# Performance work log

Hardware: AMD Instinct MI355X
Metric: run time of the kernel (lower is better)

The kernel has to match this reference:

```python
import jax, jax.numpy as jnp
import numpy as np
from jax import lax

TEMP = 65.0
CLIP_DIST = 0.01
EPS = 1e-6  # torch PairwiseDistance eps (added to the difference) and log eps
NTOKEN, NINP, NHID = 32000, 1024, 1024
SEQ_LEN, BSZ, NSAMPLES = 128, 64, 10


def setup_inputs() -> dict:
    key = jax.random.key(0)
    ks = jax.random.split(key, 7)
    data = jax.random.randint(ks[0], (SEQ_LEN, BSZ), 0, NTOKEN)
    samples = jax.random.randint(ks[1], (NSAMPLES, SEQ_LEN * BSZ), 0, NTOKEN)
    # encoder init_weights: uniform(-0.1, 0.1); RNN weights small to avoid tanh saturation
    emb_W = jax.random.uniform(ks[2], (NTOKEN, NINP), minval=-0.1, maxval=0.1, dtype=jnp.float32)
    W_ih = jax.random.normal(ks[3], (NHID, NINP), dtype=jnp.float32) * 0.03
    b_ih = jax.random.normal(ks[4], (NHID,), dtype=jnp.float32) * 0.01
    W_hh = jax.random.normal(ks[5], (NHID, NHID), dtype=jnp.float32) * 0.03
    b_hh = jax.random.normal(ks[6], (NHID,), dtype=jnp.float32) * 0.01
    return {"data": data, "samples": samples, "emb_W": emb_W,
            "W_ih": W_ih, "b_ih": b_ih, "W_hh": W_hh, "b_hh": b_hh}


def _sq_pdist(x, y):
    # torch PairwiseDistance(p=2).pow(2): ||x - y + eps||^2 (no sqrt needed)
    d = x - y + EPS
    return jnp.sum(d * d, axis=-1)


def reference(data, samples, emb_W, W_ih, b_ih, W_hh, b_hh):
    seq_len, bsz = data.shape
    nhid = W_hh.shape[0]
    emb = emb_W[data]                                  # [S, B, ninp]
    h0 = jnp.zeros((bsz, nhid), dtype=emb_W.dtype)

    def step(h, e):
        h_new = jnp.tanh(e @ W_ih.T + b_ih + h @ W_hh.T + b_hh)
        return h_new, h_new

    _, outs = lax.scan(step, h0, emb)                  # [S, B, H]
    raw = jnp.concatenate([h0[None], outs], axis=0)    # [S+1, B, H]

    # positive term: temp * ||h_t - h_{t+1}||^2, summed, averaged over seq_len
    pos = TEMP * _sq_pdist(raw[:-1], raw[1:])          # [S, B]
    loss = pos.sum() / seq_len

    prev = raw[:-1].reshape(seq_len * bsz, nhid)       # [S*B, H]
    samples_emb = emb_W[samples]                       # [ns, S*B, ninp]
    samples_W = samples_emb @ W_ih.T + b_ih            # [ns, S*B, H]
    hiddens_U = prev @ W_hh.T + b_hh                   # [S*B, H]

    out = jnp.tanh(samples_W + hiddens_U[None])        # [ns, S*B, H]
    dist = _sq_pdist(prev[None], out)                  # [ns, S*B]
    dist = jnp.clip(dist, 0.0, CLIP_DIST)
    n = seq_len * bsz
    sum_of_exp = jnp.sum(jnp.exp(-dist), axis=0) / n   # [S*B]
    loss = loss + jnp.log(sum_of_exp + EPS).sum()
    return loss
```

## Files before the change

### kernel.cpp

```cpp
#include <hip/hip_runtime.h>
#include <hip/hip_bf16.h>
#include <cmath>

typedef __bf16 bf16;
typedef __attribute__((ext_vector_type(8))) __bf16 bf16x8;
typedef __attribute__((ext_vector_type(4))) __bf16 bf16x4;
typedef __attribute__((ext_vector_type(4))) float f32x4;
typedef unsigned long long ull;

#define TEMPC 65.0f
#define EPSC 1e-6f

#define GLD_LDS16(gptr, lptr)                                                             \
    __builtin_amdgcn_global_load_lds(                                                     \
        (const __attribute__((address_space(1))) unsigned int*)(gptr),                    \
        (__attribute__((address_space(3))) unsigned int*)(lptr), 16, 0, 0)

__global__ void conv_kernel(const float* __restrict__ s, bf16* __restrict__ d, int n)
{
    int i = (blockIdx.x * blockDim.x + threadIdx.x) * 4;
    const int stride = gridDim.x * blockDim.x * 4;
    for (; i < n; i += stride) {
        const float4 v = *(const float4*)(s + i);
        bf16x4 o;
        o[0] = (bf16)v.x; o[1] = (bf16)v.y; o[2] = (bf16)v.z; o[3] = (bf16)v.w;
        *(bf16x4*)(d + i) = o;
    }
}

__global__ __launch_bounds__(256)
void pgemm_kernel(const bf16* __restrict__ A, const bf16* __restrict__ Wmat,
                  const float* __restrict__ bih, bf16* __restrict__ P)
{
    __shared__ __align__(16) bf16 As[2 * 128 * 32];
    __shared__ __align__(16) bf16 Bs[2 * 128 * 32];

    const int tid = threadIdx.x;
    const int l  = tid & 63;
    const int w  = tid >> 6;
    const int wr = w >> 1, wc = w & 1;
    const int wg = (blockIdx.x & 7) * 250 + (blockIdx.x >> 3);
    const int mbase = (wg >> 3) * 128;
    const int nbase = (wg & 7) * 128;

    const int r0 = w * 32 + (l >> 2);
    const int csw = ((l & 3) ^ ((l >> 3) & 3)) * 16;
    const char* Asrc0 = (const char*)A + (size_t)(mbase + r0) * 2048 + csw;
    const char* Asrc1 = (const char*)A + (size_t)(mbase + r0 + 16) * 2048 + csw;
    const char* Bsrc0 = (const char*)Wmat + (size_t)(nbase + r0) * 2048 + csw;
    const char* Bsrc1 = (const char*)Wmat + (size_t)(nbase + r0 + 16) * 2048 + csw;

    const int frow  = l & 15;
    const int koffE = (((l >> 4) ^ ((frow >> 1) & 3)) * 8);
    const bf16* Ard = As + (wr * 64 + frow) * 32 + koffE;
    const bf16* Brd = Bs + (wc * 64 + frow) * 32 + koffE;

    auto stage = [&](int buf, int kb) {
        bf16* As_ = As + buf * 4096 + w * 1024;
        bf16* Bs_ = Bs + buf * 4096 + w * 1024;
        GLD_LDS16(Asrc0 + kb, As_);
        GLD_LDS16(Asrc1 + kb, As_ + 512);
        GLD_LDS16(Bsrc0 + kb, Bs_);
        GLD_LDS16(Bsrc1 + kb, Bs_ + 512);
    };

    stage(0, 0);
    stage(1, 64);

    f32x4 acc[4][4] = {};
    for (int k = 0; k < 32; ++k) {
        if (k == 31) asm volatile("s_waitcnt vmcnt(0)" ::: "memory");
        else         asm volatile("s_waitcnt vmcnt(4)" ::: "memory");
        __syncthreads();
        const bf16* Ab = Ard + (k & 1) * 4096;
        const bf16* Bb = Brd + (k & 1) * 4096;
        bf16x8 af[4], bfr[4];
        #pragma unroll
        for (int mt = 0; mt < 4; ++mt) af[mt]  = *(const bf16x8*)(Ab + mt * 16 * 32);
        #pragma unroll
        for (int nt = 0; nt < 4; ++nt) bfr[nt] = *(const bf16x8*)(Bb + nt * 16 * 32);
        #pragma unroll
        for (int mt = 0; mt < 4; ++mt)
            #pragma unroll
            for (int nt = 0; nt < 4; ++nt)
                acc[mt][nt] = __builtin_amdgcn_mfma_f32_16x16x32_bf16(af[mt], bfr[nt], acc[mt][nt], 0, 0, 0);
        __syncthreads();
        if (k + 2 < 32) stage(k & 1, (k + 2) * 64);
    }

    #pragma unroll
    for (int mt = 0; mt < 4; ++mt)
        #pragma unroll
        for (int nt = 0; nt < 4; ++nt) {
            const int colg = nbase + wc * 64 + nt * 16 + frow;
            const float bi = bih[colg];
            #pragma unroll
            for (int r = 0; r < 4; ++r) {
                const int rowg = mbase + wr * 64 + mt * 16 + (l >> 4) * 4 + r;
                P[(size_t)rowg * 1024 + colg] = (bf16)(acc[mt][nt][r] + bi);
            }
        }
}

__global__ __launch_bounds__(256, 1)
void rnn_fused(const int* __restrict__ data, bf16* __restrict__ raw,
               const bf16* __restrict__ Whh, const bf16* __restrict__ P,
               const float* __restrict__ bhh, bf16* __restrict__ Ust,
               int* __restrict__ cnt)
{
    __shared__ __align__(16) bf16 Wlds[64 * 1024];
    __shared__ __align__(16) char Hlds[8 * 2064];
    __shared__ int Tlds[1024];

    const int tid    = threadIdx.x;
    const int l      = tid & 63;
    const int w      = tid >> 6;
    const int group  = blockIdx.x & 7;
    const int slot   = blockIdx.x >> 3;
    const int jbase  = slot * 64;
    const int frow   = l & 15;
    const int kchunk = l >> 4;
    const int jglob  = jbase + w * 16 + frow;
    const int rr     = frow & 7;

    for (int i = tid; i < 1024; i += 256)
        Tlds[i] = data[(i >> 3) * 64 + group * 8 + (i & 7)];

    {
        const int jloc = l >> 2;
        const int csw  = ((l & 3) ^ ((l >> 3) & 3)) * 16;
        const char* gsrc = (const char*)Whh + (size_t)(jbase + w * 16 + jloc) * 2048 + csw;
        for (int kk = 0; kk < 32; ++kk)
            GLD_LDS16(gsrc + kk * 64, Wlds + (kk * 4 + w) * 512);
        asm volatile("s_waitcnt vmcnt(0)" ::: "memory");
        __syncthreads();
    }
    const float bh = bhh[jglob];

    const int ksw   = kchunk ^ ((frow >> 1) & 3);
    const bf16* wrd = Wlds + w * 512 + frow * 32 + ksw * 8;
    const char* hrd = Hlds + rr * 2064 + kchunk * 16;

    for (int t = 0; t < 128; ++t) {
        if (t > 0) {
            if (tid < 4)
                while (__hip_atomic_load(&cnt[((t * 8 + group) * 4 + tid) * 32],
                                         __ATOMIC_RELAXED, __HIP_MEMORY_SCOPE_AGENT) < 4)
                    __builtin_amdgcn_s_sleep(1);
            __syncthreads();
        }
        const ull* hsrc8 = (const ull*)(raw + (size_t)t * 65536 + group * 8192);
        ull hv[8];
        #pragma unroll
        for (int i = 0; i < 8; ++i)
            hv[i] = __hip_atomic_load(hsrc8 + tid + i * 256,
                                      __ATOMIC_RELAXED, __HIP_MEMORY_SCOPE_AGENT);
        float xw[4];
        #pragma unroll
        for (int r = 0; r < 4; ++r) {
            const int bc  = (kchunk * 4 + r) & 7;
            const int tok = Tlds[t * 8 + bc];
            xw[r] = (float)P[(size_t)tok * 1024 + jglob];
        }
        #pragma unroll
        for (int i = 0; i < 8; ++i)
            *(ull*)(Hlds + i * 2064 + tid * 8) = hv[i];
        __syncthreads();

        f32x4 acc0 = {0.f,0.f,0.f,0.f}, acc1 = {0.f,0.f,0.f,0.f};
        #pragma unroll
        for (int kk = 0; kk < 32; kk += 2) {
            bf16x8 a0 = *(const bf16x8*)(hrd + kk * 64);
            bf16x8 a1 = *(const bf16x8*)(hrd + kk * 64 + 64);
            acc0 = __builtin_amdgcn_mfma_f32_16x16x32_bf16(a0, *(const bf16x8*)(wrd + kk * 2048),       acc0, 0, 0, 0);
            acc1 = __builtin_amdgcn_mfma_f32_16x16x32_bf16(a1, *(const bf16x8*)(wrd + (kk + 1) * 2048), acc1, 0, 0, 0);
        }

        bf16* rawN = raw + (size_t)(t + 1) * 65536;
        if (l < 32) {
            #pragma unroll
            for (int r = 0; r < 4; ++r) {
                const int b = (l >> 4) * 4 + r;
                const float V = acc0[r] + acc1[r] + bh;
                const float h = tanhf(xw[r] + V);
                const size_t row = (size_t)(t * 64 + group * 8 + b);
                Ust[row * 1024 + jglob] = (bf16)V;
                const bf16 hb = (bf16)h;
                unsigned short hs = __builtin_bit_cast(unsigned short, hb);
                unsigned short hn = (unsigned short)__shfl_down((int)hs, 1, 64);
                if ((frow & 1) == 0) {
                    unsigned int pack = (unsigned int)hs | ((unsigned int)hn << 16);
                    unsigned int* dst = (unsigned int*)(rawN + (size_t)(group * 8 + b) * 1024 + jglob);
                    __hip_atomic_store(dst, pack, __ATOMIC_RELAXED, __HIP_MEMORY_SCOPE_AGENT);
                }
            }
        }
        if (t < 127) {
            __syncthreads();
            if (tid == 0)
                __hip_atomic_fetch_add(&cnt[(((t + 1) * 8 + group) * 4 + (slot & 3)) * 32], 1,
                                       __ATOMIC_RELAXED, __HIP_MEMORY_SCOPE_AGENT);
        }
    }
}

__global__ void pos_kernel(const bf16* __restrict__ raw, float* __restrict__ lacc)
{
    float s = 0.f;
    const int NV = (128 * 64 * 1024) / 8;
    for (int i = blockIdx.x * blockDim.x + threadIdx.x; i < NV; i += gridDim.x * blockDim.x) {
        bf16x8 a = *(const bf16x8*)(raw + (size_t)i * 8);
        bf16x8 b = *(const bf16x8*)(raw + (size_t)i * 8 + 65536);
        #pragma unroll
        for (int j = 0; j < 8; ++j) {
            const float d = (float)a[j] - (float)b[j] + EPSC;
            s += d * d;
        }
    }
    #pragma unroll
    for (int off = 32; off > 0; off >>= 1) s += __shfl_down(s, off, 64);
    if ((threadIdx.x & 63) == 0) atomicAdd(lacc, s * (TEMPC / 128.f));
}

__global__ __launch_bounds__(256)
void neg_kernel(const int* __restrict__ samples, const bf16* __restrict__ P,
                const bf16* __restrict__ Ust, const bf16* __restrict__ raw,
                float* __restrict__ lacc)
{
    const int l = threadIdx.x & 63;
    const int r = blockIdx.x * 4 + (threadIdx.x >> 6);
    const bf16* u  = Ust + (size_t)r * 1024;
    const bf16* pv = raw + (size_t)r * 1024;

    float uf[16], vf[16];
    {
        bf16x8 u0 = *(const bf16x8*)(u + l * 8);
        bf16x8 u1 = *(const bf16x8*)(u + 512 + l * 8);
        bf16x8 v0 = *(const bf16x8*)(pv + l * 8);
        bf16x8 v1 = *(const bf16x8*)(pv + 512 + l * 8);
        #pragma unroll
        for (int i = 0; i < 8; ++i) {
            uf[i] = (float)u0[i]; uf[8 + i] = (float)u1[i];
            vf[i] = (float)v0[i]; vf[8 + i] = (float)v1[i];
        }
    }

    float se = 0.f;
    #pragma unroll
    for (int s = 0; s < 10; ++s) {
        const int tok = samples[s * 8192 + r];
        const bf16* pr = P + (size_t)tok * 1024;
        bf16x8 p0 = *(const bf16x8*)(pr + l * 8);
        bf16x8 p1 = *(const bf16x8*)(pr + 512 + l * 8);
        float d2 = 0.f;
        #pragma unroll
        for (int i = 0; i < 8; ++i) {
            const float o0 = tanhf((float)p0[i] + uf[i]);
            const float d0 = vf[i] - o0 + EPSC;
            d2 += d0 * d0;
            const float o1 = tanhf((float)p1[i] + uf[8 + i]);
            const float d1 = vf[8 + i] - o1 + EPSC;
            d2 += d1 * d1;
        }
        #pragma unroll
        for (int off = 1; off < 64; off <<= 1)
            d2 += __shfl_xor(d2, off, 64);
        se += expf(-fminf(d2, 0.01f));
    }
    if (l == 0) atomicAdd(lacc, logf(se * (1.f / 8192.f) + EPSC));
}

__global__ void fin_kernel(const float* __restrict__ lacc, float* __restrict__ out)
{
    if (threadIdx.x == 0) out[0] = lacc[0];
}

extern "C" void kernel_launch(void* const* d_in, const int* in_sizes, int n_in,
                              void* d_out, int out_size, void* d_ws, size_t ws_size,
                              hipStream_t stream)
{
    const int*   data    = (const int*)d_in[0];
    const int*   samples = (const int*)d_in[1];
    const float* emb     = (const float*)d_in[2];
    const float* Wih     = (const float*)d_in[3];
    const float* bih     = (const float*)d_in[4];
    const float* Whh     = (const float*)d_in[5];
    const float* bhh     = (const float*)d_in[6];

    char* ws = (char*)d_ws;
    size_t off = 0;
    auto alloc = [&](size_t bytes) { void* p = ws + off; off += (bytes + 255) & ~(size_t)255; return p; };
    bf16*  emb_b = (bf16*)alloc((size_t)32000 * 1024 * 2);
    bf16*  Wih_b = (bf16*)alloc((size_t)1024 * 1024 * 2);
    bf16*  Whh_b = (bf16*)alloc((size_t)1024 * 1024 * 2);
    bf16*  P     = (bf16*)alloc((size_t)32000 * 1024 * 2);
    bf16*  Ust   = (bf16*)alloc((size_t)8192 * 1024 * 2);
    bf16*  raw   = (bf16*)alloc((size_t)129 * 64 * 1024 * 2);
    float* lacc  = (float*)alloc(256);
    int*   cnt   = (int*)alloc(524288);

    hipMemsetAsync(raw,  0, 64 * 1024 * 2, stream);
    hipMemsetAsync(lacc, 0, 256, stream);
    hipMemsetAsync(cnt,  0, 524288, stream);

    conv_kernel<<<2048, 256, 0, stream>>>(emb, emb_b, 32000 * 1024);
    conv_kernel<<<512, 256, 0, stream>>>(Wih, Wih_b, 1024 * 1024);
    conv_kernel<<<512, 256, 0, stream>>>(Whh, Whh_b, 1024 * 1024);

    pgemm_kernel<<<2000, 256, 0, stream>>>(emb_b, Wih_b, bih, P);

    rnn_fused<<<128, 256, 0, stream>>>(data, raw, Whh_b, P, bhh, Ust, cnt);

    pos_kernel<<<512, 256, 0, stream>>>(raw, lacc);

    neg_kernel<<<2048, 256, 0, stream>>>(samples, P, Ust, raw, lacc);

    fin_kernel<<<1, 64, 0, stream>>>(lacc, (float*)d_out);
}
```

Before: 705.2 us.

## Replace RNN counter barrier with sentinel-polling on hidden state data

The inter-block step synchronization in the persistent RNN kernel no longer uses atomic counters. Instead the raw hidden-state buffer is pre-filled with 0xFF, and each thread polls its own loaded words, reloading any 16-bit lane that still holds the all-ones sentinel (a NaN pattern tanh output never produces). This drops the counter fetch_add, the spin loop and two block barriers per step, at the cost of an extra full-buffer memset and relying on the ordering of the packed 32-bit stores. The GEMM also swaps __syncthreads for raw s_barrier with an explicit lgkmcnt wait.

```diff
diff --git a/kernel.cpp b/kernel.cpp
--- a/kernel.cpp
+++ b/kernel.cpp
@@ -15,6 +15,12 @@
     __builtin_amdgcn_global_load_lds(                                                     \
         (const __attribute__((address_space(1))) unsigned int*)(gptr),                    \
         (__attribute__((address_space(3))) unsigned int*)(lptr), 16, 0, 0)
+
+__device__ __forceinline__ ull badw(ull x)
+{
+    ull y = ~x;
+    return (y - 0x0001000100010001ull) & ~y & 0x8000800080008000ull;
+}
 
 __global__ void conv_kernel(const float* __restrict__ s, bf16* __restrict__ d, int n)
 {
@@ -71,7 +77,7 @@
     for (int k = 0; k < 32; ++k) {
         if (k == 31) asm volatile("s_waitcnt vmcnt(0)" ::: "memory");
         else         asm volatile("s_waitcnt vmcnt(4)" ::: "memory");
-        __syncthreads();
+        __builtin_amdgcn_s_barrier();
         const bf16* Ab = Ard + (k & 1) * 4096;
         const bf16* Bb = Brd + (k & 1) * 4096;
         bf16x8 af[4], bfr[4];
@@ -84,7 +90,8 @@
             #pragma unroll
             for (int nt = 0; nt < 4; ++nt)
                 acc[mt][nt] = __builtin_amdgcn_mfma_f32_16x16x32_bf16(af[mt], bfr[nt], acc[mt][nt], 0, 0, 0);
-        __syncthreads();
+        asm volatile("s_waitcnt lgkmcnt(0)" ::: "memory");
+        __builtin_amdgcn_s_barrier();
         if (k + 2 < 32) stage(k & 1, (k + 2) * 64);
     }
 
@@ -105,8 +112,7 @@
 __global__ __launch_bounds__(256, 1)
 void rnn_fused(const int* __restrict__ data, bf16* __restrict__ raw,
                const bf16* __restrict__ Whh, const bf16* __restrict__ P,
-               const float* __restrict__ bhh, bf16* __restrict__ Ust,
-               int* __restrict__ cnt)
+               const float* __restrict__ bhh, bf16* __restrict__ Ust)
 {
     __shared__ __align__(16) bf16 Wlds[64 * 1024];
     __shared__ __align__(16) char Hlds[8 * 2064];
@@ -142,13 +148,6 @@
     const char* hrd = Hlds + rr * 2064 + kchunk * 16;
 
     for (int t = 0; t < 128; ++t) {
-        if (t > 0) {
-            if (tid < 4)
-                while (__hip_atomic_load(&cnt[((t * 8 + group) * 4 + tid) * 32],
-                                         __ATOMIC_RELAXED, __HIP_MEMORY_SCOPE_AGENT) < 4)
-                    __builtin_amdgcn_s_sleep(1);
-            __syncthreads();
-        }
         const ull* hsrc8 = (const ull*)(raw + (size_t)t * 65536 + group * 8192);
         ull hv[8];
         #pragma unroll
@@ -162,6 +161,18 @@
             const int tok = Tlds[t * 8 + bc];
             xw[r] = (float)P[(size_t)tok * 1024 + jglob];
         }
+        for (;;) {
+            ull anybad = 0;
+            #pragma unroll
+            for (int i = 0; i < 8; ++i) anybad |= badw(hv[i]);
+            if (!anybad) break;
+            #pragma unroll
+            for (int i = 0; i < 8; ++i)
+                if (badw(hv[i]))
+                    hv[i] = __hip_atomic_load(hsrc8 + tid + i * 256,
+                                              __ATOMIC_RELAXED, __HIP_MEMORY_SCOPE_AGENT);
+        }
+        __syncthreads();
         #pragma unroll
         for (int i = 0; i < 8; ++i)
             *(ull*)(Hlds + i * 2064 + tid * 8) = hv[i];
@@ -195,12 +206,6 @@
                 }
             }
         }
-        if (t < 127) {
-            __syncthreads();
-            if (tid == 0)
-                __hip_atomic_fetch_add(&cnt[(((t + 1) * 8 + group) * 4 + (slot & 3)) * 32], 1,
-                                       __ATOMIC_RELAXED, __HIP_MEMORY_SCOPE_AGENT);
-        }
     }
 }
 
@@ -297,11 +302,10 @@
     bf16*  Ust   = (bf16*)alloc((size_t)8192 * 1024 * 2);
     bf16*  raw   = (bf16*)alloc((size_t)129 * 64 * 1024 * 2);
     float* lacc  = (float*)alloc(256);
-    int*   cnt   = (int*)alloc(524288);
-
-    hipMemsetAsync(raw,  0, 64 * 1024 * 2, stream);
+
+    hipMemsetAsync(raw, 0xFF, (size_t)129 * 64 * 1024 * 2, stream);
+    hipMemsetAsync(raw, 0, 64 * 1024 * 2, stream);
     hipMemsetAsync(lacc, 0, 256, stream);
-    hipMemsetAsync(cnt,  0, 524288, stream);
 
     conv_kernel<<<2048, 256, 0, stream>>>(emb, emb_b, 32000 * 1024);
     conv_kernel<<<512, 256, 0, stream>>>(Wih, Wih_b, 1024 * 1024);
@@ -309,7 +313,7 @@
 
     pgemm_kernel<<<2000, 256, 0, stream>>>(emb_b, Wih_b, bih, P);
 
-    rnn_fused<<<128, 256, 0, stream>>>(data, raw, Whh_b, P, bhh, Ust, cnt);
+    rnn_fused<<<128, 256, 0, stream>>>(data, raw, Whh_b, P, bhh, Ust);
 
     pos_kernel<<<512, 256, 0, stream>>>(raw, lacc);
 
```

Result: slower. 727.9 us (+3.2%).

## Overlap full-vocab projection GEMM with the serial RNN recurrence in one launch

Applied to the files above, without the earlier changes.

A small gather-GEMM now computes the input projection for only the 8192 data tokens before the recurrence. A fused kernel runs the 128-block RNN recurrence alongside the 2000-block full-vocabulary projection GEMM, so the sequential RNN's idle compute units can do the big GEMM concurrently. The GEMM loops also swap __syncthreads for raw s_barrier with explicit lgkmcnt waits. The risk is that the RNN blocks need 147KB of LDS and spin-wait on each other, so they must all be resident at once and may contend with the GEMM blocks for memory bandwidth.

```diff
diff --git a/kernel.cpp b/kernel.cpp
--- a/kernel.cpp
+++ b/kernel.cpp
@@ -29,8 +29,9 @@
 }
 
 __global__ __launch_bounds__(256)
-void pgemm_kernel(const bf16* __restrict__ A, const bf16* __restrict__ Wmat,
-                  const float* __restrict__ bih, bf16* __restrict__ P)
+void gemm0_kernel(const int* __restrict__ idx, const bf16* __restrict__ emb,
+                  const bf16* __restrict__ Wmat, const float* __restrict__ bih,
+                  bf16* __restrict__ XWout)
 {
     __shared__ __align__(16) bf16 As[2 * 128 * 32];
     __shared__ __align__(16) bf16 Bs[2 * 128 * 32];
@@ -39,14 +40,14 @@
     const int l  = tid & 63;
     const int w  = tid >> 6;
     const int wr = w >> 1, wc = w & 1;
-    const int wg = (blockIdx.x & 7) * 250 + (blockIdx.x >> 3);
+    const int wg = (blockIdx.x & 7) * 64 + (blockIdx.x >> 3);
     const int mbase = (wg >> 3) * 128;
     const int nbase = (wg & 7) * 128;
 
     const int r0 = w * 32 + (l >> 2);
     const int csw = ((l & 3) ^ ((l >> 3) & 3)) * 16;
-    const char* Asrc0 = (const char*)A + (size_t)(mbase + r0) * 2048 + csw;
-    const char* Asrc1 = (const char*)A + (size_t)(mbase + r0 + 16) * 2048 + csw;
+    const char* Asrc0 = (const char*)emb + (size_t)idx[mbase + r0] * 2048 + csw;
+    const char* Asrc1 = (const char*)emb + (size_t)idx[mbase + r0 + 16] * 2048 + csw;
     const char* Bsrc0 = (const char*)Wmat + (size_t)(nbase + r0) * 2048 + csw;
     const char* Bsrc1 = (const char*)Wmat + (size_t)(nbase + r0 + 16) * 2048 + csw;
 
@@ -71,7 +72,7 @@
     for (int k = 0; k < 32; ++k) {
         if (k == 31) asm volatile("s_waitcnt vmcnt(0)" ::: "memory");
         else         asm volatile("s_waitcnt vmcnt(4)" ::: "memory");
-        __syncthreads();
+        __builtin_amdgcn_s_barrier();
         const bf16* Ab = Ard + (k & 1) * 4096;
         const bf16* Bb = Brd + (k & 1) * 4096;
         bf16x8 af[4], bfr[4];
@@ -84,7 +85,8 @@
             #pragma unroll
             for (int nt = 0; nt < 4; ++nt)
                 acc[mt][nt] = __builtin_amdgcn_mfma_f32_16x16x32_bf16(af[mt], bfr[nt], acc[mt][nt], 0, 0, 0);
-        __syncthreads();
+        asm volatile("s_waitcnt lgkmcnt(0)" ::: "memory");
+        __builtin_amdgcn_s_barrier();
         if (k + 2 < 32) stage(k & 1, (k + 2) * 64);
     }
 
@@ -97,110 +99,177 @@
             #pragma unroll
             for (int r = 0; r < 4; ++r) {
                 const int rowg = mbase + wr * 64 + mt * 16 + (l >> 4) * 4 + r;
-                P[(size_t)rowg * 1024 + colg] = (bf16)(acc[mt][nt][r] + bi);
+                XWout[(size_t)rowg * 1024 + colg] = (bf16)(acc[mt][nt][r] + bi);
             }
         }
 }
 
 __global__ __launch_bounds__(256, 1)
-void rnn_fused(const int* __restrict__ data, bf16* __restrict__ raw,
-               const bf16* __restrict__ Whh, const bf16* __restrict__ P,
-               const float* __restrict__ bhh, bf16* __restrict__ Ust,
-               int* __restrict__ cnt)
-{
-    __shared__ __align__(16) bf16 Wlds[64 * 1024];
-    __shared__ __align__(16) char Hlds[8 * 2064];
-    __shared__ int Tlds[1024];
-
-    const int tid    = threadIdx.x;
-    const int l      = tid & 63;
-    const int w      = tid >> 6;
-    const int group  = blockIdx.x & 7;
-    const int slot   = blockIdx.x >> 3;
-    const int jbase  = slot * 64;
-    const int frow   = l & 15;
-    const int kchunk = l >> 4;
-    const int jglob  = jbase + w * 16 + frow;
-    const int rr     = frow & 7;
-
-    for (int i = tid; i < 1024; i += 256)
-        Tlds[i] = data[(i >> 3) * 64 + group * 8 + (i & 7)];
-
-    {
-        const int jloc = l >> 2;
-        const int csw  = ((l & 3) ^ ((l >> 3) & 3)) * 16;
-        const char* gsrc = (const char*)Whh + (size_t)(jbase + w * 16 + jloc) * 2048 + csw;
-        for (int kk = 0; kk < 32; ++kk)
-            GLD_LDS16(gsrc + kk * 64, Wlds + (kk * 4 + w) * 512);
-        asm volatile("s_waitcnt vmcnt(0)" ::: "memory");
-        __syncthreads();
-    }
-    const float bh = bhh[jglob];
-
-    const int ksw   = kchunk ^ ((frow >> 1) & 3);
-    const bf16* wrd = Wlds + w * 512 + frow * 32 + ksw * 8;
-    const char* hrd = Hlds + rr * 2064 + kchunk * 16;
-
-    for (int t = 0; t < 128; ++t) {
-        if (t > 0) {
-            if (tid < 4)
-                while (__hip_atomic_load(&cnt[((t * 8 + group) * 4 + tid) * 32],
-                                         __ATOMIC_RELAXED, __HIP_MEMORY_SCOPE_AGENT) < 4)
-                    __builtin_amdgcn_s_sleep(1);
+void fused_kernel(const bf16* __restrict__ emb, const bf16* __restrict__ Wih,
+                  const float* __restrict__ bih, bf16* __restrict__ P,
+                  bf16* __restrict__ raw, const bf16* __restrict__ Whh,
+                  const bf16* __restrict__ XWb, const float* __restrict__ bhh,
+                  bf16* __restrict__ Ust, int* __restrict__ cnt)
+{
+    __shared__ __align__(16) char pool[147584];
+    const int tid = threadIdx.x;
+    const int l   = tid & 63;
+    const int w   = tid >> 6;
+    const int id  = blockIdx.x;
+
+    if (id < 128) {
+        bf16* Wlds = (bf16*)pool;
+        char* Hlds = pool + 131072;
+        const int group  = id & 7;
+        const int slot   = id >> 3;
+        const int jbase  = slot * 64;
+        const int frow   = l & 15;
+        const int kchunk = l >> 4;
+        const int jglob  = jbase + w * 16 + frow;
+        const int rr     = frow & 7;
+
+        {
+            const int jloc = l >> 2;
+            const int csw  = ((l & 3) ^ ((l >> 3) & 3)) * 16;
+            const char* gsrc = (const char*)Whh + (size_t)(jbase + w * 16 + jloc) * 2048 + csw;
+            for (int kk = 0; kk < 32; ++kk)
+                GLD_LDS16(gsrc + kk * 64, Wlds + (kk * 4 + w) * 512);
+            asm volatile("s_waitcnt vmcnt(0)" ::: "memory");
             __syncthreads();
         }
-        const ull* hsrc8 = (const ull*)(raw + (size_t)t * 65536 + group * 8192);
-        ull hv[8];
-        #pragma unroll
-        for (int i = 0; i < 8; ++i)
-            hv[i] = __hip_atomic_load(hsrc8 + tid + i * 256,
-                                      __ATOMIC_RELAXED, __HIP_MEMORY_SCOPE_AGENT);
-        float xw[4];
-        #pragma unroll
-        for (int r = 0; r < 4; ++r) {
-            const int bc  = (kchunk * 4 + r) & 7;
-            const int tok = Tlds[t * 8 + bc];
-            xw[r] = (float)P[(size_t)tok * 1024 + jglob];
-        }
-        #pragma unroll
-        for (int i = 0; i < 8; ++i)
-            *(ull*)(Hlds + i * 2064 + tid * 8) = hv[i];
-        __syncthreads();
-
-        f32x4 acc0 = {0.f,0.f,0.f,0.f}, acc1 = {0.f,0.f,0.f,0.f};
-        #pragma unroll
-        for (int kk = 0; kk < 32; kk += 2) {
-            bf16x8 a0 = *(const bf16x8*)(hrd + kk * 64);
-            bf16x8 a1 = *(const bf16x8*)(hrd + kk * 64 + 64);
-            acc0 = __builtin_amdgcn_mfma_f32_16x16x32_bf16(a0, *(const bf16x8*)(wrd + kk * 2048),       acc0, 0, 0, 0);
-            acc1 = __builtin_amdgcn_mfma_f32_16x16x32_bf16(a1, *(const bf16x8*)(wrd + (kk + 1) * 2048), acc1, 0, 0, 0);
-        }
-
-        bf16* rawN = raw + (size_t)(t + 1) * 65536;
-        if (l < 32) {
+        const float bh = bhh[jglob];
+
+        const int ksw   = kchunk ^ ((frow >> 1) & 3);
+        const bf16* wrd = Wlds + w * 512 + frow * 32 + ksw * 8;
+        const char* hrd = Hlds + rr * 2064 + kchunk * 16;
+
+        for (int t = 0; t < 128; ++t) {
+            if (t > 0) {
+                if (tid < 4)
+                    while (__hip_atomic_load(&cnt[((t * 8 + group) * 4 + tid) * 32],
+                                             __ATOMIC_RELAXED, __HIP_MEMORY_SCOPE_AGENT) < 4)
+                        __builtin_amdgcn_s_sleep(1);
+                __syncthreads();
+            }
+            const ull* hsrc8 = (const ull*)(raw + (size_t)t * 65536 + group * 8192);
+            ull hv[8];
+            #pragma unroll
+            for (int i = 0; i < 8; ++i)
+                hv[i] = __hip_atomic_load(hsrc8 + tid + i * 256,
+                                          __ATOMIC_RELAXED, __HIP_MEMORY_SCOPE_AGENT);
+            float xw[4];
             #pragma unroll
             for (int r = 0; r < 4; ++r) {
-                const int b = (l >> 4) * 4 + r;
-                const float V = acc0[r] + acc1[r] + bh;
-                const float h = tanhf(xw[r] + V);
-                const size_t row = (size_t)(t * 64 + group * 8 + b);
-                Ust[row * 1024 + jglob] = (bf16)V;
-                const bf16 hb = (bf16)h;
-                unsigned short hs = __builtin_bit_cast(unsigned short, hb);
-                unsigned short hn = (unsigned short)__shfl_down((int)hs, 1, 64);
-                if ((frow & 1) == 0) {
-                    unsigned int pack = (unsigned int)hs | ((unsigned int)hn << 16);
-                    unsigned int* dst = (unsigned int*)(rawN + (size_t)(group * 8 + b) * 1024 + jglob);
-                    __hip_atomic_store(dst, pack, __ATOMIC_RELAXED, __HIP_MEMORY_SCOPE_AGENT);
+                const int bc = (kchunk * 4 + r) & 7;
+                xw[r] = (float)XWb[(size_t)(t * 64 + group * 8 + bc) * 1024 + jglob];
+            }
+            #pragma unroll
+            for (int i = 0; i < 8; ++i)
+                *(ull*)(Hlds + i * 2064 + tid * 8) = hv[i];
+            __syncthreads();
+
+            f32x4 acc0 = {0.f,0.f,0.f,0.f}, acc1 = {0.f,0.f,0.f,0.f};
+            #pragma unroll
+            for (int kk = 0; kk < 32; kk += 2) {
+                bf16x8 a0 = *(const bf16x8*)(hrd + kk * 64);
+                bf16x8 a1 = *(const bf16x8*)(hrd + kk * 64 + 64);
+                acc0 = __builtin_amdgcn_mfma_f32_16x16x32_bf16(a0, *(const bf16x8*)(wrd + kk * 2048),       acc0, 0, 0, 0);
+                acc1 = __builtin_amdgcn_mfma_f32_16x16x32_bf16(a1, *(const bf16x8*)(wrd + (kk + 1) * 2048), acc1, 0, 0, 0);
+            }
+
+            bf16* rawN = raw + (size_t)(t + 1) * 65536;
+            if (l < 32) {
+                #pragma unroll
+                for (int r = 0; r < 4; ++r) {
+                    const int b = (l >> 4) * 4 + r;
+                    const float V = acc0[r] + acc1[r] + bh;
+                    const float h = tanhf(xw[r] + V);
+                    const size_t row = (size_t)(t * 64 + group * 8 + b);
+                    Ust[row * 1024 + jglob] = (bf16)V;
+                    const bf16 hb = (bf16)h;
+                    unsigned short hs = __builtin_bit_cast(unsigned short, hb);
+                    unsigned short hn = (unsigned short)__shfl_down((int)hs, 1, 64);
+                    if ((frow & 1) == 0) {
+                        unsigned int pack = (unsigned int)hs | ((unsigned int)hn << 16);
+                        unsigned int* dst = (unsigned int*)(rawN + (size_t)(group * 8 + b) * 1024 + jglob);
+                        __hip_atomic_store(dst, pack, __ATOMIC_RELAXED, __HIP_MEMORY_SCOPE_AGENT);
+                    }
                 }
             }
-        }
-        if (t < 127) {
-            __syncthreads();
-            if (tid == 0)
-                __hip_atomic_fetch_add(&cnt[(((t + 1) * 8 + group) * 4 + (slot & 3)) * 32], 1,
-                                       __ATOMIC_RELAXED, __HIP_MEMORY_SCOPE_AGENT);
-        }
+            if (t < 127) {
+                __syncthreads();
+                if (tid == 0)
+                    __hip_atomic_fetch_add(&cnt[(((t + 1) * 8 + group) * 4 + (slot & 3)) * 32], 1,
+                                           __ATOMIC_RELAXED, __HIP_MEMORY_SCOPE_AGENT);
+            }
+        }
+    } else {
+        bf16* As = (bf16*)pool;
+        bf16* Bs = (bf16*)(pool + 16384);
+        const int q  = id - 128;
+        const int wg = (q & 7) * 250 + (q >> 3);
+        const int mbase = (wg >> 3) * 128;
+        const int nbase = (wg & 7) * 128;
+        const int wr = w >> 1, wc = w & 1;
+
+        const int r0 = w * 32 + (l >> 2);
+        const int csw = ((l & 3) ^ ((l >> 3) & 3)) * 16;
+        const char* Asrc0 = (const char*)emb + (size_t)(mbase + r0) * 2048 + csw;
+        const char* Asrc1 = (const char*)emb + (size_t)(mbase + r0 + 16) * 2048 + csw;
+        const char* Bsrc0 = (const char*)Wih + (size_t)(nbase + r0) * 2048 + csw;
+        const char* Bsrc1 = (const char*)Wih + (size_t)(nbase + r0 + 16) * 2048 + csw;
+
+        const int frow  = l & 15;
+        const int koffE = (((l >> 4) ^ ((frow >> 1) & 3)) * 8);
+        const bf16* Ard = As + (wr * 64 + frow) * 32 + koffE;
+        const bf16* Brd = Bs + (wc * 64 + frow) * 32 + koffE;
+
+        auto stage = [&](int buf, int kb) {
+            bf16* As_ = As + buf * 4096 + w * 1024;
+            bf16* Bs_ = Bs + buf * 4096 + w * 1024;
+            GLD_LDS16(Asrc0 + kb, As_);
+            GLD_LDS16(Asrc1 + kb, As_ + 512);
+            GLD_LDS16(Bsrc0 + kb, Bs_);
+            GLD_LDS16(Bsrc1 + kb, Bs_ + 512);
+        };
+
+        stage(0, 0);
+        stage(1, 64);
+
+        f32x4 acc[4][4] = {};
+        for (int k = 0; k < 32; ++k) {
+            if (k == 31) asm volatile("s_waitcnt vmcnt(0)" ::: "memory");
+            else         asm volatile("s_waitcnt vmcnt(4)" ::: "memory");
+            __builtin_amdgcn_s_barrier();
+            const bf16* Ab = Ard + (k & 1) * 4096;
+            const bf16* Bb = Brd + (k & 1) * 4096;
+            bf16x8 af[4], bfr[4];
+            #pragma unroll
+            for (int mt = 0; mt < 4; ++mt) af[mt]  = *(const bf16x8*)(Ab + mt * 16 * 32);
+            #pragma unroll
+            for (int nt = 0; nt < 4; ++nt) bfr[nt] = *(const bf16x8*)(Bb + nt * 16 * 32);
+            #pragma unroll
+            for (int mt = 0; mt < 4; ++mt)
+                #pragma unroll
+                for (int nt = 0; nt < 4; ++nt)
+                    acc[mt][nt] = __builtin_amdgcn_mfma_f32_16x16x32_bf16(af[mt], bfr[nt], acc[mt][nt], 0, 0, 0);
+            asm volatile("s_waitcnt lgkmcnt(0)" ::: "memory");
+            __builtin_amdgcn_s_barrier();
+            if (k + 2 < 32) stage(k & 1, (k + 2) * 64);
+        }
+
+        #pragma unroll
+        for (int mt = 0; mt < 4; ++mt)
+            #pragma unroll
+            for (int nt = 0; nt < 4; ++nt) {
+                const int colg = nbase + wc * 64 + nt * 16 + frow;
+                const float bi = bih[colg];
+                #pragma unroll
+                for (int r = 0; r < 4; ++r) {
+                    const int rowg = mbase + wr * 64 + mt * 16 + (l >> 4) * 4 + r;
+                    P[(size_t)rowg * 1024 + colg] = (bf16)(acc[mt][nt][r] + bi);
+                }
+            }
     }
 }
 
@@ -294,12 +363,13 @@
     bf16*  Wih_b = (bf16*)alloc((size_t)1024 * 1024 * 2);
     bf16*  Whh_b = (bf16*)alloc((size_t)1024 * 1024 * 2);
     bf16*  P     = (bf16*)alloc((size_t)32000 * 1024 * 2);
+    bf16*  XWb   = (bf16*)alloc((size_t)8192 * 1024 * 2);
     bf16*  Ust   = (bf16*)alloc((size_t)8192 * 1024 * 2);
     bf16*  raw   = (bf16*)alloc((size_t)129 * 64 * 1024 * 2);
     float* lacc  = (float*)alloc(256);
     int*   cnt   = (int*)alloc(524288);
 
-    hipMemsetAsync(raw,  0, 64 * 1024 * 2, stream);
+    hipMemsetAsync(raw, 0, 64 * 1024 * 2, stream);
     hipMemsetAsync(lacc, 0, 256, stream);
     hipMemsetAsync(cnt,  0, 524288, stream);
 
@@ -307,9 +377,10 @@
     conv_kernel<<<512, 256, 0, stream>>>(Wih, Wih_b, 1024 * 1024);
     conv_kernel<<<512, 256, 0, stream>>>(Whh, Whh_b, 1024 * 1024);
 
-    pgemm_kernel<<<2000, 256, 0, stream>>>(emb_b, Wih_b, bih, P);
-
-    rnn_fused<<<128, 256, 0, stream>>>(data, raw, Whh_b, P, bhh, Ust, cnt);
+    gemm0_kernel<<<512, 256, 0, stream>>>(data, emb_b, Wih_b, bih, XWb);
+
+    fused_kernel<<<2128, 256, 0, stream>>>(emb_b, Wih_b, bih, P,
+                                           raw, Whh_b, XWb, bhh, Ust, cnt);
 
     pos_kernel<<<512, 256, 0, stream>>>(raw, lacc);
 
```

New measurement: 665.3 us. 1.06x faster.
